# Kernel optimization log

Hardware: AMD Instinct MI355X
Metric: run time of the kernel (lower is better)

## Reference

```python
import jax, jax.numpy as jnp
import numpy as np

N_ATOMS = 50000
N_EDGES = 1600000
DIM = 128
N_FILTERS = 128
OUT_DIM = 128
N_GAUSS = 50
CUTOFF = 10.0
LOG2 = float(np.log(2.0))


def ssp(x):
    # ShiftedSoftplus: softplus(x) - log(2)
    return jax.nn.softplus(x) - LOG2


def setup_inputs() -> dict:
    key = jax.random.key(0)
    ks = jax.random.split(key, 10)
    inp = {}
    inp["x"] = jax.random.normal(ks[0], (N_ATOMS, DIM), dtype=jnp.float32)
    inp["r_ij"] = jax.random.uniform(ks[1], (N_EDGES,), dtype=jnp.float32) * CUTOFF
    inp["f_ij"] = jax.random.normal(ks[2], (N_EDGES, N_GAUSS), dtype=jnp.float32)
    inp["ind_i"] = jax.random.randint(ks[3], (N_EDGES,), 0, N_ATOMS)
    inp["ind_j"] = jax.random.randint(ks[4], (N_EDGES,), 0, N_ATOMS)
    # filter network: Linear(50,128) + SSP + Linear(128,128) + SSP
    inp["Wf1"] = jax.random.normal(ks[5], (N_GAUSS, N_FILTERS), dtype=jnp.float32) / np.sqrt(N_GAUSS)
    inp["bf1"] = jnp.zeros((N_FILTERS,), dtype=jnp.float32)
    inp["Wf2"] = jax.random.normal(ks[6], (N_FILTERS, N_FILTERS), dtype=jnp.float32) / np.sqrt(N_FILTERS)
    inp["bf2"] = jnp.zeros((N_FILTERS,), dtype=jnp.float32)
    # in2f: Linear(dim, n_filters, bias=False)
    inp["Win"] = jax.random.normal(ks[7], (DIM, N_FILTERS), dtype=jnp.float32) / np.sqrt(DIM)
    # f2out: Linear(n_filters, out_dim) + SSP
    inp["Wout"] = jax.random.normal(ks[8], (N_FILTERS, OUT_DIM), dtype=jnp.float32) / np.sqrt(N_FILTERS)
    inp["bout"] = jnp.zeros((OUT_DIM,), dtype=jnp.float32)
    return inp


def reference(x, r_ij, f_ij, ind_i, ind_j, Wf1, bf1, Wf2, bf2, Win, Wout, bout):
    # filter network on edge features: [E, n_gauss] -> [E, n_filters]
    W = ssp(f_ij @ Wf1 + bf1)
    W = ssp(W @ Wf2 + bf2)
    # cosine cutoff: [E]
    C = 0.5 * (jnp.cos(r_ij * (jnp.pi / CUTOFF)) + 1.0)
    C = C * (r_ij < CUTOFF).astype(C.dtype)
    W = W * C[:, None]
    # node projection: [N, dim] -> [N, n_filters]
    h = x @ Win
    # gather neighbor features, apply filter, scatter-add by ind_i
    m = h[ind_j] * W                                   # [E, n_filters]
    agg = jax.ops.segment_sum(m, ind_i, num_segments=x.shape[0])  # [N, n_filters]
    # f2out: Linear + ShiftedSoftplus
    return ssp(agg @ Wout + bout)
```

## Files before the change

### kernel.cpp

```cpp
#include <hip/hip_runtime.h>
#include <math.h>

#define N_ATOMS 50000
#define N_EDGES 1600000
#define NF 128
#define NG 50
#define ITERS 4
#define EPB 512
#define LOG2F_ 0.69314718055994530942f
#define PI_OVER_CUT 0.31415926535897932f
#define CUTOFF_F 10.0f

typedef _Float16 half_t;
typedef _Float16 f16x8 __attribute__((ext_vector_type(8)));
typedef _Float16 f16x2 __attribute__((ext_vector_type(2)));
typedef float f32x4 __attribute__((ext_vector_type(4)));
typedef unsigned int u32x4 __attribute__((ext_vector_type(4)));

__device__ __forceinline__ float sspf_fast(float x) {
    float e = __expf(-fabsf(x));
    float l = __logf(1.0f + e);
    return fmaxf(x, 0.0f) + (l - LOG2F_);
}

__device__ __forceinline__ unsigned short f2h_bits(float x) {
    half_t h = (half_t)x;
    return __builtin_bit_cast(unsigned short, h);
}

template <bool BIAS_SSP>
__global__ __launch_bounds__(256) void gemm128_kernel(
    const float* __restrict__ X, const float* __restrict__ W,
    const float* __restrict__ bias, float* __restrict__ Y, int N) {
    __shared__ float xs[32][128];
    const int row0 = blockIdx.x * 32;
    const int tid = threadIdx.x;
    {
        const float4* src = (const float4*)(X + (size_t)row0 * 128);
        float4* dst = (float4*)(&xs[0][0]);
        for (int i = tid; i < 32 * 32; i += 256) {
            int r = i >> 5;
            float4 v = {0.f, 0.f, 0.f, 0.f};
            if (row0 + r < N) v = src[i];
            dst[i] = v;
        }
    }
    __syncthreads();

    const int rq = tid >> 5;
    const int cq = tid & 31;
    float4 a0 = {0,0,0,0}, a1 = {0,0,0,0}, a2 = {0,0,0,0}, a3 = {0,0,0,0};
    const float4* Wv = (const float4*)W;

    #pragma unroll 4
    for (int k = 0; k < 128; ++k) {
        float4 w = Wv[k * 32 + cq];
        float x0 = xs[rq * 4 + 0][k];
        float x1 = xs[rq * 4 + 1][k];
        float x2 = xs[rq * 4 + 2][k];
        float x3 = xs[rq * 4 + 3][k];
        a0.x += x0 * w.x; a0.y += x0 * w.y; a0.z += x0 * w.z; a0.w += x0 * w.w;
        a1.x += x1 * w.x; a1.y += x1 * w.y; a1.z += x1 * w.z; a1.w += x1 * w.w;
        a2.x += x2 * w.x; a2.y += x2 * w.y; a2.z += x2 * w.z; a2.w += x2 * w.w;
        a3.x += x3 * w.x; a3.y += x3 * w.y; a3.z += x3 * w.z; a3.w += x3 * w.w;
    }

    float4 bq = {0,0,0,0};
    if (BIAS_SSP) bq = ((const float4*)bias)[cq];
    #pragma unroll
    for (int i = 0; i < 4; ++i) {
        float4 v = (i == 0) ? a0 : (i == 1) ? a1 : (i == 2) ? a2 : a3;
        int r = row0 + rq * 4 + i;
        if (r >= N) continue;
        if (BIAS_SSP) {
            v.x = sspf_fast(v.x + bq.x); v.y = sspf_fast(v.y + bq.y);
            v.z = sspf_fast(v.z + bq.z); v.w = sspf_fast(v.w + bq.w);
        }
        ((float4*)(Y + (size_t)r * 128))[cq] = v;
    }
}

__global__ __launch_bounds__(256) void preconv_kernel(
    const float* __restrict__ Wf1, const float* __restrict__ Wf2,
    half_t* __restrict__ w1t, half_t* __restrict__ w2t) {
    int id = blockIdx.x * 256 + threadIdx.x;
    if (id < 128 * 64) {
        int col = id >> 6, k = id & 63;
        w1t[id] = (k < NG) ? (half_t)Wf1[k * NF + col] : (half_t)0.0f;
    } else if (id < 128 * 64 + 128 * 128) {
        int t = id - 128 * 64;
        int col = t >> 7, k = t & 127;
        w2t[t] = (half_t)Wf2[k * NF + col];
    }
}

#define OFF_W2T   16384
#define OFF_W1OUT 49152

__global__ __launch_bounds__(512, 4) void edge_kernel(
    const float* __restrict__ f_ij, const float* __restrict__ r_ij,
    const int* __restrict__ ind_i, const int* __restrict__ ind_j,
    const half_t* __restrict__ w1t_g, const half_t* __restrict__ w2t_g,
    const float* __restrict__ bf1, const float* __restrict__ bf2,
    const float* __restrict__ h, float* __restrict__ agg) {
    __shared__ __align__(16) unsigned char lds[81920];
    const int tid = threadIdx.x;

    for (int c = tid; c < 1024; c += 512) {
        int col = c >> 3, kc = c & 7;
        u32x4 v = ((const u32x4*)w1t_g)[c];
        *(u32x4*)(lds + (col << 7) + ((kc ^ (col & 7)) << 4)) = v;
    }
    for (int c = tid; c < 2048; c += 512) {
        int col = c >> 4, kc = c & 15;
        u32x4 v = ((const u32x4*)w2t_g)[c];
        int slot = (kc & 8) | ((kc & 7) ^ (col & 7));
        *(u32x4*)(lds + OFF_W2T + (col << 8) + (slot << 4)) = v;
    }

    const int lane = tid & 63;
    const int wid = tid >> 6;
    const int l15 = lane & 15;
    const int lg  = lane >> 4;
    const int l7  = lane & 7;
    const int h3  = l15 >> 3;
    const int hb  = (l7 >> 2) & 1;
    const int lgl = lg ^ (l7 & 3);

    float b1r[8], b2r[8];
    #pragma unroll
    for (int t = 0; t < 8; ++t) {
        b1r[t] = bf1[t * 16 + l15];
        b2r[t] = bf2[t * 16 + l15];
    }

    const int b1b0 = (l15 << 7) + (hb << 6) + (lgl << 4);
    const int b1b1 = (l15 << 7) + ((hb ^ 1) << 6) + (lgl << 4);
    const int b2b0 = OFF_W2T + (l15 << 8) + (hb << 6) + (lgl << 4);
    const int b2b1 = OFF_W2T + (l15 << 8) + ((hb ^ 1) << 6) + (lgl << 4);
    const int a2b0 = OFF_W1OUT + wid * 4096 + (l15 << 8) + (hb << 6) + (lgl << 4);
    const int a2b1 = OFF_W1OUT + wid * 4096 + (l15 << 8) + ((hb ^ 1) << 6) + (lgl << 4);
    const int ep1base = OFF_W1OUT + wid * 4096 + lg * 1024 + l7 * 2;
    const int rw4 = (lg & 1) * 4;

    const int bb = blockIdx.x * EPB;
    const float* aptr = f_ij + (size_t)(bb + wid * 16 + l15) * NG + lg * 8;

    __syncthreads();

    for (int it = 0; it < ITERS; ++it) {
        const int eb = bb + it * 128 + wid * 16;
        const int erow = eb + lg * 4;

        float rv[4]; int jv[4], iv[4];
        #pragma unroll
        for (int r = 0; r < 4; ++r) {
            rv[r] = r_ij[erow + r];
            jv[r] = ind_j[erow + r];
            iv[r] = ind_i[erow + r];
        }

        float2 q[8];
        #pragma unroll
        for (int p = 0; p < 4; ++p) q[p] = *(const float2*)(aptr + 2 * p);
        #pragma unroll
        for (int p = 0; p < 4; ++p) {
            float2 v = {0.f, 0.f};
            if (lg * 8 + 2 * p <= 16) v = *(const float2*)(aptr + 32 + 2 * p);
            q[4 + p] = v;
        }
        aptr += (size_t)128 * NG;

        float hv[4][8];
        #pragma unroll
        for (int r = 0; r < 4; ++r) {
            const float* hrow = h + (size_t)jv[r] * NF + l15;
            #pragma unroll
            for (int t = 0; t < 8; ++t) hv[r][t] = hrow[t * 16];
        }

        f16x8 a1[2];
        #pragma unroll
        for (int ks = 0; ks < 2; ++ks) {
            #pragma unroll
            for (int p = 0; p < 4; ++p) {
                f16x2 hvv = __builtin_bit_cast(f16x2,
                    __builtin_amdgcn_cvt_pkrtz(q[ks * 4 + p].x, q[ks * 4 + p].y));
                a1[ks][2 * p]     = hvv[0];
                a1[ks][2 * p + 1] = hvv[1];
            }
        }

        f32x4 acc1[8];
        #pragma unroll
        for (int t = 0; t < 8; ++t) acc1[t] = (f32x4){0.f, 0.f, 0.f, 0.f};
        #pragma unroll
        for (int t = 0; t < 8; ++t) {
            f16x8 b0 = *(const f16x8*)(lds + b1b0 + t * 2048);
            f16x8 b1 = *(const f16x8*)(lds + b1b1 + t * 2048);
            acc1[t] = __builtin_amdgcn_mfma_f32_16x16x32_f16(a1[0], b0, acc1[t], 0, 0, 0);
            acc1[t] = __builtin_amdgcn_mfma_f32_16x16x32_f16(a1[1], b1, acc1[t], 0, 0, 0);
        }

        #pragma unroll
        for (int t = 0; t < 8; ++t) {
            #pragma unroll
            for (int r = 0; r < 4; ++r) {
                unsigned short bits = f2h_bits(sspf_fast(acc1[t][r] + b1r[t]));
                int slotx = (2 * (t & 3) + h3) ^ (rw4 + r);
                *(unsigned short*)(lds + ep1base + r * 256 + ((t >> 2) << 7) + (slotx << 4)) = bits;
            }
        }

        f32x4 acc2[8];
        #pragma unroll
        for (int t = 0; t < 8; ++t) acc2[t] = (f32x4){0.f, 0.f, 0.f, 0.f};
        f16x8 a2[4];
        #pragma unroll
        for (int ks = 0; ks < 4; ++ks) {
            int addr = ((ks & 1) ? a2b1 : a2b0) + (ks >> 1) * 128;
            a2[ks] = *(const f16x8*)(lds + addr);
        }
        #pragma unroll
        for (int t = 0; t < 8; ++t) {
            #pragma unroll
            for (int ks = 0; ks < 4; ++ks) {
                int addr = ((ks & 1) ? b2b1 : b2b0) + (ks >> 1) * 128 + t * 4096;
                f16x8 b = *(const f16x8*)(lds + addr);
                acc2[t] = __builtin_amdgcn_mfma_f32_16x16x32_f16(a2[ks], b, acc2[t], 0, 0, 0);
            }
        }

        #pragma unroll
        for (int r = 0; r < 4; ++r) {
            float c = 0.5f * (__cosf(rv[r] * PI_OVER_CUT) + 1.0f);
            c = (rv[r] < CUTOFF_F) ? c : 0.0f;
            float* grow = agg + (size_t)iv[r] * NF + l15;
            #pragma unroll
            for (int t = 0; t < 8; ++t) {
                float w2 = sspf_fast(acc2[t][r] + b2r[t]) * c;
                atomicAdd(grow + t * 16, hv[r][t] * w2);
            }
        }
    }
}

extern "C" void kernel_launch(void* const* d_in, const int* in_sizes, int n_in,
                              void* d_out, int out_size, void* d_ws, size_t ws_size,
                              hipStream_t stream) {
    const float* x     = (const float*)d_in[0];
    const float* r_ij  = (const float*)d_in[1];
    const float* f_ij  = (const float*)d_in[2];
    const int*   ind_i = (const int*)d_in[3];
    const int*   ind_j = (const int*)d_in[4];
    const float* Wf1   = (const float*)d_in[5];
    const float* bf1   = (const float*)d_in[6];
    const float* Wf2   = (const float*)d_in[7];
    const float* bf2   = (const float*)d_in[8];
    const float* Win   = (const float*)d_in[9];
    const float* Wout  = (const float*)d_in[10];
    const float* bout  = (const float*)d_in[11];
    float* out = (float*)d_out;

    float*  agg  = (float*)d_ws;
    float*  h    = agg + (size_t)N_ATOMS * NF;
    half_t* w1t  = (half_t*)(h + (size_t)N_ATOMS * NF);
    half_t* w2t  = w1t + 128 * 64;

    (void)hipMemsetAsync(agg, 0, (size_t)N_ATOMS * NF * sizeof(float), stream);

    preconv_kernel<<<96, 256, 0, stream>>>(Wf1, Wf2, w1t, w2t);

    const int gemm_blocks = (N_ATOMS + 31) / 32;
    gemm128_kernel<false><<<gemm_blocks, 256, 0, stream>>>(x, Win, nullptr, h, N_ATOMS);

    edge_kernel<<<N_EDGES / EPB, 512, 0, stream>>>(f_ij, r_ij, ind_i, ind_j,
                                                   w1t, w2t, bf1, bf2, h, agg);

    gemm128_kernel<true><<<gemm_blocks, 256, 0, stream>>>(agg, Wout, bout, out, N_ATOMS);
}
```

Baseline: 757.0 us.

## Store node features and aggregation buffer in fp16 with packed atomic adds

The node projection h and the aggregation buffer agg are now stored in fp16 instead of fp32. The edge kernel gathers packed half pairs, exchanges filter weights between neighbouring lanes with a shuffle, and scatters with global_atomic_pk_add_f16, so each atomic updates two channels. This halves the gather and atomic traffic and the number of atomic instructions. In exchange, about 32 fp16 atomic accumulations per node lose precision, which may exceed the accuracy tolerance.

```diff
diff --git a/kernel.cpp b/kernel.cpp
--- a/kernel.cpp
+++ b/kernel.cpp
@@ -28,15 +28,29 @@
     return __builtin_bit_cast(unsigned short, h);
 }
 
-template <bool BIAS_SSP>
+__device__ __forceinline__ unsigned int pk2(float a, float b) {
+    return __builtin_bit_cast(unsigned int, __builtin_amdgcn_cvt_pkrtz(a, b));
+}
+
+template <bool BIAS_SSP, bool IN_HALF, bool OUT_HALF>
 __global__ __launch_bounds__(256) void gemm128_kernel(
-    const float* __restrict__ X, const float* __restrict__ W,
-    const float* __restrict__ bias, float* __restrict__ Y, int N) {
+    const void* __restrict__ Xv, const float* __restrict__ W,
+    const float* __restrict__ bias, void* __restrict__ Yv, int N) {
     __shared__ float xs[32][128];
     const int row0 = blockIdx.x * 32;
     const int tid = threadIdx.x;
-    {
-        const float4* src = (const float4*)(X + (size_t)row0 * 128);
+
+    if (IN_HALF) {
+        const half_t* X = (const half_t*)Xv;
+        for (int i = tid; i < 32 * 16; i += 256) {
+            int r = i >> 4;
+            f16x8 v = {0, 0, 0, 0, 0, 0, 0, 0};
+            if (row0 + r < N) v = *((const f16x8*)(X + (size_t)row0 * 128) + i);
+            #pragma unroll
+            for (int e = 0; e < 8; ++e) xs[r][(i & 15) * 8 + e] = (float)v[e];
+        }
+    } else {
+        const float4* src = (const float4*)((const float*)Xv + (size_t)row0 * 128);
         float4* dst = (float4*)(&xs[0][0]);
         for (int i = tid; i < 32 * 32; i += 256) {
             int r = i >> 5;
@@ -76,7 +90,12 @@
             v.x = sspf_fast(v.x + bq.x); v.y = sspf_fast(v.y + bq.y);
             v.z = sspf_fast(v.z + bq.z); v.w = sspf_fast(v.w + bq.w);
         }
-        ((float4*)(Y + (size_t)r * 128))[cq] = v;
+        if (OUT_HALF) {
+            uint2 st = { pk2(v.x, v.y), pk2(v.z, v.w) };
+            *(uint2*)((half_t*)Yv + (size_t)r * 128 + cq * 4) = st;
+        } else {
+            ((float4*)((float*)Yv + (size_t)r * 128))[cq] = v;
+        }
     }
 }
 
@@ -102,7 +121,7 @@
     const int* __restrict__ ind_i, const int* __restrict__ ind_j,
     const half_t* __restrict__ w1t_g, const half_t* __restrict__ w2t_g,
     const float* __restrict__ bf1, const float* __restrict__ bf2,
-    const float* __restrict__ h, float* __restrict__ agg) {
+    const half_t* __restrict__ h, half_t* __restrict__ agg) {
     __shared__ __align__(16) unsigned char lds[81920];
     const int tid = threadIdx.x;
 
@@ -126,6 +145,7 @@
     const int h3  = l15 >> 3;
     const int hb  = (l7 >> 2) & 1;
     const int lgl = lg ^ (l7 & 3);
+    const int par = lane & 1;
 
     float b1r[8], b2r[8];
     #pragma unroll
@@ -171,12 +191,13 @@
         }
         aptr += (size_t)128 * NG;
 
-        float hv[4][8];
+        unsigned int hd[4][4];
         #pragma unroll
         for (int r = 0; r < 4; ++r) {
-            const float* hrow = h + (size_t)jv[r] * NF + l15;
-            #pragma unroll
-            for (int t = 0; t < 8; ++t) hv[r][t] = hrow[t * 16];
+            const unsigned int* hrow = (const unsigned int*)(h + (size_t)jv[r] * NF);
+            #pragma unroll
+            for (int u = 0; u < 4; ++u)
+                hd[r][u] = hrow[(par ? (4 + u) * 8 : u * 8) + (l15 >> 1)];
         }
 
         f16x8 a1[2];
@@ -235,11 +256,22 @@
         for (int r = 0; r < 4; ++r) {
             float c = 0.5f * (__cosf(rv[r] * PI_OVER_CUT) + 1.0f);
             c = (rv[r] < CUTOFF_F) ? c : 0.0f;
-            float* grow = agg + (size_t)iv[r] * NF + l15;
-            #pragma unroll
-            for (int t = 0; t < 8; ++t) {
-                float w2 = sspf_fast(acc2[t][r] + b2r[t]) * c;
-                atomicAdd(grow + t * 16, hv[r][t] * w2);
+            float w2v[8];
+            #pragma unroll
+            for (int t = 0; t < 8; ++t) w2v[t] = sspf_fast(acc2[t][r] + b2r[t]) * c;
+            half_t* arow = agg + (size_t)iv[r] * NF;
+            #pragma unroll
+            for (int u = 0; u < 4; ++u) {
+                float send = par ? w2v[u] : w2v[4 + u];
+                float recv = __shfl_xor(send, 1);
+                float wA = par ? recv : w2v[u];
+                float wB = par ? w2v[4 + u] : recv;
+                f16x2 hp = __builtin_bit_cast(f16x2, hd[r][u]);
+                unsigned int pk = pk2((float)hp[0] * wA, (float)hp[1] * wB);
+                int t = par ? 4 + u : u;
+                half_t* ap = arow + t * 16 + (l15 & ~1);
+                asm volatile("global_atomic_pk_add_f16 %0, %1, off"
+                             :: "v"(ap), "v"(pk) : "memory");
             }
         }
     }
@@ -262,20 +294,22 @@
     const float* bout  = (const float*)d_in[11];
     float* out = (float*)d_out;
 
-    float*  agg  = (float*)d_ws;
-    float*  h    = agg + (size_t)N_ATOMS * NF;
-    half_t* w1t  = (half_t*)(h + (size_t)N_ATOMS * NF);
-    half_t* w2t  = w1t + 128 * 64;
-
-    (void)hipMemsetAsync(agg, 0, (size_t)N_ATOMS * NF * sizeof(float), stream);
+    half_t* agg = (half_t*)d_ws;
+    half_t* h   = agg + (size_t)N_ATOMS * NF;
+    half_t* w1t = h + (size_t)N_ATOMS * NF;
+    half_t* w2t = w1t + 128 * 64;
+
+    (void)hipMemsetAsync(agg, 0, (size_t)N_ATOMS * NF * sizeof(half_t), stream);
 
     preconv_kernel<<<96, 256, 0, stream>>>(Wf1, Wf2, w1t, w2t);
 
     const int gemm_blocks = (N_ATOMS + 31) / 32;
-    gemm128_kernel<false><<<gemm_blocks, 256, 0, stream>>>(x, Win, nullptr, h, N_ATOMS);
+    gemm128_kernel<false, false, true><<<gemm_blocks, 256, 0, stream>>>(
+        x, Win, nullptr, h, N_ATOMS);
 
     edge_kernel<<<N_EDGES / EPB, 512, 0, stream>>>(f_ij, r_ij, ind_i, ind_j,
                                                    w1t, w2t, bf1, bf2, h, agg);
 
-    gemm128_kernel<true><<<gemm_blocks, 256, 0, stream>>>(agg, Wout, bout, out, N_ATOMS);
-}
+    gemm128_kernel<true, true, false><<<gemm_blocks, 256, 0, stream>>>(
+        agg, Wout, bout, out, N_ATOMS);
+}
```

Result: slower. 773.8 us (+2.2%).

## Software-pipeline edge metadata and f_ij loads across iterations, relax occupancy bound

Applied to the files above, without the earlier changes.

Prefetches the next iteration's r_ij, ind_i, ind_j and f_ij rows into registers while the current iteration runs its MFMA and epilogue work, and fully unrolls the iteration loop. The goal is to hide global load latency behind compute. Because this needs more registers, the launch bound drops from 4 to 3 blocks per CU, which lowers occupancy and so reduces the hardware's own latency hiding.

```diff
diff --git a/kernel.cpp b/kernel.cpp
--- a/kernel.cpp
+++ b/kernel.cpp
@@ -97,7 +97,7 @@
 #define OFF_W2T   16384
 #define OFF_W1OUT 49152
 
-__global__ __launch_bounds__(512, 4) void edge_kernel(
+__global__ __launch_bounds__(512, 3) void edge_kernel(
     const float* __restrict__ f_ij, const float* __restrict__ r_ij,
     const int* __restrict__ ind_i, const int* __restrict__ ind_j,
     const half_t* __restrict__ w1t_g, const half_t* __restrict__ w2t_g,
@@ -148,29 +148,28 @@
 
     __syncthreads();
 
-    for (int it = 0; it < ITERS; ++it) {
-        const int eb = bb + it * 128 + wid * 16;
-        const int erow = eb + lg * 4;
-
-        float rv[4]; int jv[4], iv[4];
+    float rv[4]; int jv[4], iv[4];
+    {
+        const int erow = bb + wid * 16 + lg * 4;
         #pragma unroll
         for (int r = 0; r < 4; ++r) {
             rv[r] = r_ij[erow + r];
             jv[r] = ind_j[erow + r];
             iv[r] = ind_i[erow + r];
         }
-
-        float2 q[8];
-        #pragma unroll
-        for (int p = 0; p < 4; ++p) q[p] = *(const float2*)(aptr + 2 * p);
-        #pragma unroll
-        for (int p = 0; p < 4; ++p) {
-            float2 v = {0.f, 0.f};
-            if (lg * 8 + 2 * p <= 16) v = *(const float2*)(aptr + 32 + 2 * p);
-            q[4 + p] = v;
-        }
-        aptr += (size_t)128 * NG;
-
+    }
+    float2 q[8];
+    #pragma unroll
+    for (int p = 0; p < 4; ++p) q[p] = *(const float2*)(aptr + 2 * p);
+    #pragma unroll
+    for (int p = 0; p < 4; ++p) {
+        float2 v = {0.f, 0.f};
+        if (lg * 8 + 2 * p <= 16) v = *(const float2*)(aptr + 32 + 2 * p);
+        q[4 + p] = v;
+    }
+
+    #pragma unroll
+    for (int it = 0; it < ITERS; ++it) {
         float hv[4][8];
         #pragma unroll
         for (int r = 0; r < 4; ++r) {
@@ -202,6 +201,26 @@
             acc1[t] = __builtin_amdgcn_mfma_f32_16x16x32_f16(a1[1], b1, acc1[t], 0, 0, 0);
         }
 
+        float rvN[4]; int jvN[4], ivN[4]; float2 qN[8];
+        if (it + 1 < ITERS) {
+            const int erowN = bb + (it + 1) * 128 + wid * 16 + lg * 4;
+            #pragma unroll
+            for (int r = 0; r < 4; ++r) {
+                rvN[r] = r_ij[erowN + r];
+                jvN[r] = ind_j[erowN + r];
+                ivN[r] = ind_i[erowN + r];
+            }
+            const float* aptrN = aptr + (size_t)128 * NG;
+            #pragma unroll
+            for (int p = 0; p < 4; ++p) qN[p] = *(const float2*)(aptrN + 2 * p);
+            #pragma unroll
+            for (int p = 0; p < 4; ++p) {
+                float2 v = {0.f, 0.f};
+                if (lg * 8 + 2 * p <= 16) v = *(const float2*)(aptrN + 32 + 2 * p);
+                qN[4 + p] = v;
+            }
+        }
+
         #pragma unroll
         for (int t = 0; t < 8; ++t) {
             #pragma unroll
@@ -241,6 +260,14 @@
                 float w2 = sspf_fast(acc2[t][r] + b2r[t]) * c;
                 atomicAdd(grow + t * 16, hv[r][t] * w2);
             }
+        }
+
+        if (it + 1 < ITERS) {
+            #pragma unroll
+            for (int r = 0; r < 4; ++r) { rv[r] = rvN[r]; jv[r] = jvN[r]; iv[r] = ivN[r]; }
+            #pragma unroll
+            for (int p = 0; p < 8; ++p) q[p] = qN[p];
+            aptr += (size_t)128 * NG;
         }
     }
 }
```

New measurement: 816.4 us. 7.9% more time.
